# Performance work log

Measured on AMD Instinct MI355X. Metric: run time of the kernel, lower is better.

## Reference

```python
import jax, jax.numpy as jnp
import numpy as np

D_MODEL = 1024
N_HEAD = 16
D_FF = 4 * D_MODEL
LN_EPS = 1e-5


def _layernorm(x, g, b):
    mu = jnp.mean(x, axis=-1, keepdims=True)
    var = jnp.mean(jnp.square(x - mu), axis=-1, keepdims=True)
    return (x - mu) * jax.lax.rsqrt(var + LN_EPS) * g + b


def _mha(q_in, k_in, v_in, mask, wq, bq, wk, wv, bv, wo, bo):
    B, Tq, D = q_in.shape
    H, Dk = N_HEAD, D // N_HEAD
    q = (q_in @ wq + bq).reshape(B, Tq, H, Dk).transpose(0, 2, 1, 3)      # [B,H,Tq,Dk]
    k = (k_in @ wk).reshape(B, -1, H, Dk).transpose(0, 2, 1, 3)           # [B,H,Tk,Dk]
    v = (v_in @ wv + bv).reshape(B, -1, H, Dk).transpose(0, 2, 1, 3)      # [B,H,Tk,Dk]
    attn = jnp.einsum('bhqd,bhkd->bhqk', q, k) / jnp.sqrt(jnp.float32(Dk))
    if mask is not None:
        m0 = (mask[:, None, :, :] == 0)                                    # [B,1,Tq,Tk]
        attn = jnp.where(m0, -jnp.inf, attn)
        attn = jax.nn.softmax(attn, axis=-1)
        attn = jnp.where(m0, 0.0, attn)
    else:
        attn = jax.nn.softmax(attn, axis=-1)
    out = jnp.einsum('bhqk,bhkd->bhqd', attn, v)
    out = out.transpose(0, 2, 1, 3).reshape(B, Tq, D)
    return out @ wo + bo


def setup_inputs() -> dict:
    key = jax.random.key(0)
    ks = jax.random.split(key, 32)
    B, T, S, D = 4, 1024, 1024, D_MODEL
    w = lambda k, shp: 0.02 * jax.random.normal(k, shp, dtype=jnp.float32)
    inp = {
        'dec_input': jax.random.normal(ks[0], (B, T, D), dtype=jnp.float32),
        'enc_output': jax.random.normal(ks[1], (B, S, D), dtype=jnp.float32),
        'self_mask': jnp.broadcast_to(jnp.tril(jnp.ones((T, T), jnp.int32)), (B, T, T)),
        'cross_mask': jnp.ones((B, T, S), jnp.int32),
        'sa_ln_g': jnp.ones((D,), jnp.float32), 'sa_ln_b': jnp.zeros((D,), jnp.float32),
        'sa_wq': w(ks[2], (D, D)), 'sa_bq': jnp.zeros((D,), jnp.float32),
        'sa_wk': w(ks[3], (D, D)),
        'sa_wv': w(ks[4], (D, D)), 'sa_bv': jnp.zeros((D,), jnp.float32),
        'sa_wo': w(ks[5], (D, D)), 'sa_bo': jnp.zeros((D,), jnp.float32),
        'ca_ln_g': jnp.ones((D,), jnp.float32), 'ca_ln_b': jnp.zeros((D,), jnp.float32),
        'ca_wq': w(ks[6], (D, D)), 'ca_bq': jnp.zeros((D,), jnp.float32),
        'ca_wk': w(ks[7], (D, D)),
        'ca_wv': w(ks[8], (D, D)), 'ca_bv': jnp.zeros((D,), jnp.float32),
        'ca_wo': w(ks[9], (D, D)), 'ca_bo': jnp.zeros((D,), jnp.float32),
        'mlp_ln_g': jnp.ones((D,), jnp.float32), 'mlp_ln_b': jnp.zeros((D,), jnp.float32),
        'w1': w(ks[10], (D, D_FF)), 'b1': jnp.zeros((D_FF,), jnp.float32),
        'w2': w(ks[11], (D_FF, D)), 'b2': jnp.zeros((D,), jnp.float32),
    }
    return inp


def reference(dec_input, enc_output, self_mask, cross_mask,
              sa_ln_g, sa_ln_b, sa_wq, sa_bq, sa_wk, sa_wv, sa_bv, sa_wo, sa_bo,
              ca_ln_g, ca_ln_b, ca_wq, ca_bq, ca_wk, ca_wv, ca_bv, ca_wo, ca_bo,
              mlp_ln_g, mlp_ln_b, w1, b1, w2, b2):
    # self-attention block (pre-norm, residual)
    x = _layernorm(dec_input, sa_ln_g, sa_ln_b)
    x = dec_input + _mha(x, x, x, self_mask, sa_wq, sa_bq, sa_wk, sa_wv, sa_bv, sa_wo, sa_bo)
    # cross-attention block
    h = _layernorm(x, ca_ln_g, ca_ln_b)
    x = x + _mha(h, enc_output, enc_output, cross_mask, ca_wq, ca_bq, ca_wk, ca_wv, ca_bv, ca_wo, ca_bo)
    # GELU FFN block
    h = _layernorm(x, mlp_ln_g, mlp_ln_b)
    x = x + (jax.nn.gelu(h @ w1 + b1, approximate=False) @ w2 + b2)
    return x
```

## Files before the change

kernel.cpp:

```cpp
#include <hip/hip_runtime.h>
#include <math.h>

typedef unsigned short u16;
typedef unsigned int   u32;
typedef __attribute__((ext_vector_type(8))) short bf16x8;
typedef __attribute__((ext_vector_type(4))) float f32x4;

__device__ __forceinline__ u16 f2bf(float f) {
  u32 u = __builtin_bit_cast(u32, f);
  u += 0x7fffu + ((u >> 16) & 1u);
  return (u16)(u >> 16);
}

__device__ __forceinline__ void g2l16(const u16* g, u16* l) {
  __builtin_amdgcn_global_load_lds(
      (const __attribute__((address_space(1))) unsigned int*)g,
      (__attribute__((address_space(3))) unsigned int*)l, 16, 0, 0);
}

struct TC8 { const float* s[8]; u16* d[8]; };
__global__ __launch_bounds__(256)
void transcvt8_kernel(TC8 p) {
  const float* __restrict__ W = p.s[blockIdx.z];
  u16* __restrict__ Wt = p.d[blockIdx.z];
  __shared__ float tile[32][33];
  const int n0 = blockIdx.x * 32, k0 = blockIdx.y * 32;
  const int tx = threadIdx.x & 31, ty = threadIdx.x >> 5;
  for (int i = 0; i < 4; ++i)
    tile[ty + 8 * i][tx] = W[(size_t)(k0 + ty + 8 * i) * 1024 + n0 + tx];
  __syncthreads();
  for (int i = 0; i < 4; ++i)
    Wt[(size_t)(n0 + ty + 8 * i) * 1024 + k0 + tx] = f2bf(tile[tx][ty + 8 * i]);
}

__global__ __launch_bounds__(256)
void transcvt_kernel(const float* __restrict__ W, u16* __restrict__ Wt, int K, int N) {
  __shared__ float tile[32][33];
  const int n0 = blockIdx.x * 32, k0 = blockIdx.y * 32;
  const int tx = threadIdx.x & 31, ty = threadIdx.x >> 5;
  for (int i = 0; i < 4; ++i)
    tile[ty + 8 * i][tx] = W[(size_t)(k0 + ty + 8 * i) * N + n0 + tx];
  __syncthreads();
  for (int i = 0; i < 4; ++i)
    Wt[(size_t)(n0 + ty + 8 * i) * K + k0 + tx] = f2bf(tile[tx][ty + 8 * i]);
}

__global__ __launch_bounds__(256)
void cvt_kernel(const float* __restrict__ in, u16* __restrict__ out) {
  const int i = blockIdx.x * 256 + threadIdx.x;
  const float4 v = ((const float4*)in)[i];
  u16 o[4] = {f2bf(v.x), f2bf(v.y), f2bf(v.z), f2bf(v.w)};
  ((ushort4*)out)[i] = *(ushort4*)o;
}

__global__ __launch_bounds__(256)
void pack_bias_kernel(const float* __restrict__ bq, const float* __restrict__ bv,
                      const float* __restrict__ cbv,
                      float* __restrict__ B3, float* __restrict__ B2) {
  const int i = blockIdx.x * 256 + threadIdx.x;
  if (i < 3072) {
    float v = 0.0f;
    if (i < 1024) v = bq[i];
    else if (i >= 2048) v = bv[i - 2048];
    B3[i] = v;
  } else {
    const int j = i - 3072;
    B2[j] = (j >= 1024) ? cbv[j - 1024] : 0.0f;
  }
}

__global__ __launch_bounds__(256)
void ln_kernel(const float* __restrict__ x, const float* __restrict__ g,
               const float* __restrict__ b, u16* __restrict__ out) {
  const int row = blockIdx.x;
  const float4 v4 = ((const float4*)(x + (size_t)row * 1024))[threadIdx.x];
  float vv[4] = {v4.x, v4.y, v4.z, v4.w};
  float s = vv[0] + vv[1] + vv[2] + vv[3];
  float s2 = vv[0] * vv[0] + vv[1] * vv[1] + vv[2] * vv[2] + vv[3] * vv[3];
  for (int m = 1; m < 64; m <<= 1) { s += __shfl_xor(s, m); s2 += __shfl_xor(s2, m); }
  __shared__ float ss[4], ss2[4];
  const int w = threadIdx.x >> 6;
  if ((threadIdx.x & 63) == 0) { ss[w] = s; ss2[w] = s2; }
  __syncthreads();
  s = ss[0] + ss[1] + ss[2] + ss[3];
  s2 = ss2[0] + ss2[1] + ss2[2] + ss2[3];
  const float mu = s * (1.0f / 1024.0f);
  const float var = s2 * (1.0f / 1024.0f) - mu * mu;
  const float r = rsqrtf(var + 1e-5f);
  const int c = threadIdx.x * 4;
  const float4 g4 = ((const float4*)g)[threadIdx.x];
  const float4 b4 = ((const float4*)b)[threadIdx.x];
  float gg[4] = {g4.x, g4.y, g4.z, g4.w};
  float bb[4] = {b4.x, b4.y, b4.z, b4.w};
  u16 o[4];
  for (int j = 0; j < 4; ++j) o[j] = f2bf((vv[j] - mu) * r * gg[j] + bb[j]);
  ((ushort4*)(out + (size_t)row * 1024 + c))[0] = *(ushort4*)o;
}

template<bool RES_F32, bool GELU>
__global__ __launch_bounds__(512)
void gemm_kernel(const u16* __restrict__ A, const u16* __restrict__ Bt,
                 const float* __restrict__ bias, const float* __restrict__ res,
                 void* __restrict__ Cout, int M, int N, int K) {
  __shared__ u16 As[2][128][32];
  __shared__ u16 Bs[2][128][32];
  const int t = threadIdx.x, lane = t & 63, w = t >> 6;
  const int wr = w >> 2, wc = w & 3;
  const int nwg = gridDim.x * gridDim.y;
  int bid = blockIdx.y * gridDim.x + blockIdx.x;
  bid = (bid & 7) * (nwg >> 3) + (bid >> 3);
  const int m0 = (bid / gridDim.x) * 128, n0 = (bid % gridDim.x) * 128;
  const int fr = lane & 15, fg = lane >> 4;
  const int srow = lane >> 2, scol = (lane & 3) * 8;
  const u16* Ag = &A[(size_t)(m0 + w * 16 + srow) * K + scol];
  const u16* Bg = &Bt[(size_t)(n0 + w * 16 + srow) * K + scol];
  f32x4 acc[4][2] = {};
  g2l16(Ag, &As[0][w * 16][0]);
  g2l16(Bg, &Bs[0][w * 16][0]);
  __syncthreads();
  int cur = 0;
  for (int k0 = 0; k0 < K; k0 += 32) {
    if (k0 + 32 < K) {
      const int nx = cur ^ 1, kn = k0 + 32;
      g2l16(Ag + kn, &As[nx][w * 16][0]);
      g2l16(Bg + kn, &Bs[nx][w * 16][0]);
    }
    bf16x8 af[4], bfr[2];
    for (int m = 0; m < 4; ++m) af[m] = *(bf16x8*)&As[cur][wr * 64 + m * 16 + fr][fg * 8];
    for (int n = 0; n < 2; ++n) bfr[n] = *(bf16x8*)&Bs[cur][wc * 32 + n * 16 + fr][fg * 8];
    __builtin_amdgcn_s_setprio(1);
    for (int m = 0; m < 4; ++m)
      for (int n = 0; n < 2; ++n)
        acc[m][n] = __builtin_amdgcn_mfma_f32_16x16x32_bf16(af[m], bfr[n], acc[m][n], 0, 0, 0);
    __builtin_amdgcn_s_setprio(0);
    __syncthreads();
    cur ^= 1;
  }
  for (int m = 0; m < 4; ++m)
    for (int n = 0; n < 2; ++n) {
      const int col = n0 + wc * 32 + n * 16 + fr;
      const float bv = bias ? bias[col] : 0.0f;
      for (int i = 0; i < 4; ++i) {
        const int row = m0 + wr * 64 + m * 16 + fg * 4 + i;
        float v = acc[m][n][i] + bv;
        if (GELU) v = 0.5f * v * (1.0f + erff(v * 0.70710678118654752f));
        if (RES_F32)
          ((float*)Cout)[(size_t)row * N + col] = res[(size_t)row * N + col] + v;
        else
          ((u16*)Cout)[(size_t)row * N + col] = f2bf(v);
      }
    }
}

template<bool CAUSAL>
__global__ __launch_bounds__(256)
void attn_kernel(const u16* __restrict__ Q, int ldq,
                 const u16* __restrict__ K, int ldk,
                 const u16* __restrict__ V, int ldv,
                 u16* __restrict__ O) {
  __shared__ u16 VsT[64][72];
  __shared__ u16 Ps[4][16][72];
  const int bh = blockIdx.y, b = bh >> 4, h = bh & 15;
  const int q0 = blockIdx.x * 64;
  const int t = threadIdx.x;
  const int w = t >> 6, lane = t & 63;
  const int fr = lane & 15, fg = lane >> 4;
  const int qr = q0 + w * 16;
  const int hcol = h * 64;
  const size_t qrow = (size_t)(b * 1024 + qr + fr);
  bf16x8 qf[2];
  qf[0] = *(const bf16x8*)&Q[qrow * ldq + hcol + fg * 8];
  qf[1] = *(const bf16x8*)&Q[qrow * ldq + hcol + 32 + fg * 8];
  f32x4 o[4] = {};
  float mrow[4], lrow[4] = {};
  for (int i = 0; i < 4; ++i) mrow[i] = -1e30f;
  const int vp = t >> 3, vc8 = (t & 7) * 8;
  const int nkt = CAUSAL ? (blockIdx.x + 1) : 16;
  for (int kt = 0; kt < nkt; ++kt) {
    const int k0 = kt * 64;
    {
      const bf16x8 va = *(const bf16x8*)&V[(size_t)(b * 1024 + k0 + 2 * vp) * ldv + hcol + vc8];
      const bf16x8 vb = *(const bf16x8*)&V[(size_t)(b * 1024 + k0 + 2 * vp + 1) * ldv + hcol + vc8];
      #pragma unroll
      for (int j = 0; j < 8; ++j) {
        u16 pair[2] = {((const u16*)&va)[j], ((const u16*)&vb)[j]};
        *(u32*)&VsT[vc8 + j][2 * vp] = *(u32*)pair;
      }
    }
    __syncthreads();
    f32x4 s[4] = {};
    {
      #pragma unroll
      for (int kk = 0; kk < 2; ++kk) {
        bf16x8 kf[4];
        #pragma unroll
        for (int j = 0; j < 4; ++j)
          kf[j] = *(const bf16x8*)&K[(size_t)(b * 1024 + k0 + j * 16 + fr) * ldk + hcol + kk * 32 + fg * 8];
        __builtin_amdgcn_s_setprio(1);
        #pragma unroll
        for (int j = 0; j < 4; ++j)
          s[j] = __builtin_amdgcn_mfma_f32_16x16x32_bf16(qf[kk], kf[j], s[j], 0, 0, 0);
        __builtin_amdgcn_s_setprio(0);
      }
    }
    float p[4][4], rm[4];
    const bool domask = CAUSAL && (kt == nkt - 1);
    for (int i = 0; i < 4; ++i) rm[i] = -1e30f;
    #pragma unroll
    for (int j = 0; j < 4; ++j)
      for (int i = 0; i < 4; ++i) {
        float a = s[j][i] * 0.125f;
        if (domask) {
          const int myq = qr + fg * 4 + i;
          if (k0 + j * 16 + fr > myq) a = -1e30f;
        }
        p[j][i] = a;
        rm[i] = fmaxf(rm[i], a);
      }
    for (int off = 1; off < 16; off <<= 1)
      for (int i = 0; i < 4; ++i) rm[i] = fmaxf(rm[i], __shfl_xor(rm[i], off));
    float rs[4];
    for (int i = 0; i < 4; ++i) {
      const float mn = fmaxf(mrow[i], rm[i]);
      const float sc = __expf(mrow[i] - mn);
      float acc = 0.0f;
      #pragma unroll
      for (int j = 0; j < 4; ++j) { p[j][i] = __expf(p[j][i] - mn); acc += p[j][i]; }
      mrow[i] = mn;
      lrow[i] *= sc;
      rs[i] = acc;
      for (int nb = 0; nb < 4; ++nb) o[nb][i] *= sc;
    }
    for (int off = 1; off < 16; off <<= 1)
      for (int i = 0; i < 4; ++i) rs[i] += __shfl_xor(rs[i], off);
    for (int i = 0; i < 4; ++i) {
      lrow[i] += rs[i];
      #pragma unroll
      for (int j = 0; j < 4; ++j) Ps[w][fg * 4 + i][j * 16 + fr] = f2bf(p[j][i]);
    }
    __syncthreads();
    {
      const bf16x8 pa0 = *(bf16x8*)&Ps[w][fr][fg * 8];
      const bf16x8 pa1 = *(bf16x8*)&Ps[w][fr][32 + fg * 8];
      __builtin_amdgcn_s_setprio(1);
      #pragma unroll
      for (int nb = 0; nb < 4; ++nb) {
        const bf16x8 v0 = *(const bf16x8*)&VsT[nb * 16 + fr][fg * 8];
        const bf16x8 v1 = *(const bf16x8*)&VsT[nb * 16 + fr][32 + fg * 8];
        o[nb] = __builtin_amdgcn_mfma_f32_16x16x32_bf16(pa0, v0, o[nb], 0, 0, 0);
        o[nb] = __builtin_amdgcn_mfma_f32_16x16x32_bf16(pa1, v1, o[nb], 0, 0, 0);
      }
      __builtin_amdgcn_s_setprio(0);
    }
    __syncthreads();
  }
  for (int i = 0; i < 4; ++i) {
    const float inv = 1.0f / lrow[i];
    const size_t row = (size_t)(b * 1024 + qr + fg * 4 + i);
    for (int nb = 0; nb < 4; ++nb)
      O[row * 1024 + hcol + nb * 16 + fr] = f2bf(o[nb][i] * inv);
  }
}

extern "C" void kernel_launch(void* const* d_in, const int* in_sizes, int n_in,
                              void* d_out, int out_size, void* d_ws, size_t ws_size,
                              hipStream_t stream) {
  const float* dec  = (const float*)d_in[0];
  const float* enc  = (const float*)d_in[1];
  const float* sa_g = (const float*)d_in[4];
  const float* sa_b = (const float*)d_in[5];
  const float* sa_wq = (const float*)d_in[6];
  const float* sa_bq = (const float*)d_in[7];
  const float* sa_wk = (const float*)d_in[8];
  const float* sa_wv = (const float*)d_in[9];
  const float* sa_bv = (const float*)d_in[10];
  const float* sa_wo = (const float*)d_in[11];
  const float* sa_bo = (const float*)d_in[12];
  const float* ca_g = (const float*)d_in[13];
  const float* ca_b = (const float*)d_in[14];
  const float* ca_wq = (const float*)d_in[15];
  const float* ca_bq = (const float*)d_in[16];
  const float* ca_wk = (const float*)d_in[17];
  const float* ca_wv = (const float*)d_in[18];
  const float* ca_bv = (const float*)d_in[19];
  const float* ca_wo = (const float*)d_in[20];
  const float* ca_bo = (const float*)d_in[21];
  const float* mlp_g = (const float*)d_in[22];
  const float* mlp_b = (const float*)d_in[23];
  const float* w1 = (const float*)d_in[24];
  const float* b1 = (const float*)d_in[25];
  const float* w2 = (const float*)d_in[26];
  const float* b2 = (const float*)d_in[27];

  const size_t MB = 1024 * 1024;
  if (ws_size < 97 * MB) return;
  char* ws = (char*)d_ws;
  u16* WQKV = (u16*)(ws + 0 * MB);
  u16* CQT  = (u16*)(ws + 6 * MB);
  u16* CKV  = (u16*)(ws + 8 * MB);
  u16* WOT  = (u16*)(ws + 12 * MB);
  u16* COT  = (u16*)(ws + 14 * MB);
  float* B3 = (float*)(ws + 16 * MB);
  float* B2 = (float*)(ws + 16 * MB + 16384);
  u16* XLN  = (u16*)(ws + 17 * MB);
  u16* AO   = (u16*)(ws + 25 * MB);
  u16* W1T  = (u16*)(ws + 25 * MB);
  u16* ENC  = (u16*)(ws + 33 * MB);
  u16* FB   = (u16*)(ws + 41 * MB);
  u16* EF   = (u16*)(ws + 41 * MB);
  u16* CQB  = (u16*)(ws + 57 * MB);
  u16* H1   = (u16*)(ws + 33 * MB);
  float* X1 = (float*)(ws + 65 * MB);
  u16* W2T  = (u16*)(ws + 65 * MB);
  float* X2 = (float*)(ws + 81 * MB);
  float* OUT = (float*)d_out;

  const dim3 blk(256), gblk(512);
  TC8 tc;
  tc.s[0] = sa_wq; tc.d[0] = WQKV;
  tc.s[1] = sa_wk; tc.d[1] = WQKV + 1024 * 1024;
  tc.s[2] = sa_wv; tc.d[2] = WQKV + 2048 * 1024;
  tc.s[3] = sa_wo; tc.d[3] = WOT;
  tc.s[4] = ca_wq; tc.d[4] = CQT;
  tc.s[5] = ca_wk; tc.d[5] = CKV;
  tc.s[6] = ca_wv; tc.d[6] = CKV + 1024 * 1024;
  tc.s[7] = ca_wo; tc.d[7] = COT;
  transcvt8_kernel<<<dim3(32, 32, 8), blk, 0, stream>>>(tc);
  pack_bias_kernel<<<dim3(20), blk, 0, stream>>>(sa_bq, sa_bv, ca_bv, B3, B2);
  cvt_kernel<<<dim3(4096), blk, 0, stream>>>(enc, ENC);

  ln_kernel<<<dim3(4096), blk, 0, stream>>>(dec, sa_g, sa_b, XLN);
  gemm_kernel<false, false><<<dim3(24, 32), gblk, 0, stream>>>(XLN, WQKV, B3, nullptr, FB, 4096, 3072, 1024);
  attn_kernel<true><<<dim3(16, 64), blk, 0, stream>>>(FB, 3072, FB + 1024, 3072, FB + 2048, 3072, AO);
  gemm_kernel<true, false><<<dim3(8, 32), gblk, 0, stream>>>(AO, WOT, sa_bo, dec, X1, 4096, 1024, 1024);

  ln_kernel<<<dim3(4096), blk, 0, stream>>>(X1, ca_g, ca_b, XLN);
  gemm_kernel<false, false><<<dim3(16, 32), gblk, 0, stream>>>(ENC, CKV, B2, nullptr, EF, 4096, 2048, 1024);
  gemm_kernel<false, false><<<dim3(8, 32), gblk, 0, stream>>>(XLN, CQT, ca_bq, nullptr, CQB, 4096, 1024, 1024);
  attn_kernel<false><<<dim3(16, 64), blk, 0, stream>>>(CQB, 1024, EF, 2048, EF + 1024, 2048, AO);
  gemm_kernel<true, false><<<dim3(8, 32), gblk, 0, stream>>>(AO, COT, ca_bo, X1, X2, 4096, 1024, 1024);

  transcvt_kernel<<<dim3(128, 32), blk, 0, stream>>>(w1, W1T, 1024, 4096);
  transcvt_kernel<<<dim3(32, 128), blk, 0, stream>>>(w2, W2T, 4096, 1024);
  ln_kernel<<<dim3(4096), blk, 0, stream>>>(X2, mlp_g, mlp_b, XLN);
  gemm_kernel<false, true><<<dim3(32, 32), gblk, 0, stream>>>(XLN, W1T, b1, nullptr, H1, 4096, 4096, 1024);
  gemm_kernel<true, false><<<dim3(8, 32), gblk, 0, stream>>>(H1, W2T, b2, X2, OUT, 4096, 1024, 4096);
}
```

Before: 455.9 us.

## Restructure attention kernel with double-buffered V, transposed S, and lazy softmax rescale

Rewrites the attention inner loop. The S=QK^T MFMA is computed transposed so each lane owns one query row, which removes the per-row shuffle reductions. V is double-buffered in swizzled LDS with the next tile prefetched into registers during compute, and one barrier per iteration replaces two. The softmax now uses exp2 with a folded scale, skips the rescale when the running max grows by no more than 8, and packs P stores as u32. This cuts synchronization and shuffle overhead, at the cost of more LDS and registers and some subtle lane-mapping correctness risk.

```diff
diff --git a/kernel.cpp b/kernel.cpp
--- a/kernel.cpp
+++ b/kernel.cpp
@@ -10,6 +10,9 @@
   u32 u = __builtin_bit_cast(u32, f);
   u += 0x7fffu + ((u >> 16) & 1u);
   return (u16)(u >> 16);
+}
+__device__ __forceinline__ u32 pack2(float a, float b) {
+  return (u32)f2bf(a) | ((u32)f2bf(b) << 16);
 }
 
 __device__ __forceinline__ void g2l16(const u16* g, u16* l) {
@@ -158,107 +161,132 @@
                  const u16* __restrict__ K, int ldk,
                  const u16* __restrict__ V, int ldv,
                  u16* __restrict__ O) {
-  __shared__ u16 VsT[64][72];
+  __shared__ u16 VsT[2][64][64];
   __shared__ u16 Ps[4][16][72];
   const int bh = blockIdx.y, b = bh >> 4, h = bh & 15;
   const int q0 = blockIdx.x * 64;
-  const int t = threadIdx.x;
-  const int w = t >> 6, lane = t & 63;
-  const int fr = lane & 15, fg = lane >> 4;
+  const int t = threadIdx.x, w = t >> 6, lane = t & 63;
+  const int ql = lane & 15;
+  const int hi = lane >> 4;
   const int qr = q0 + w * 16;
+  const int qz = qr + ql;
   const int hcol = h * 64;
-  const size_t qrow = (size_t)(b * 1024 + qr + fr);
-  bf16x8 qf[2];
-  qf[0] = *(const bf16x8*)&Q[qrow * ldq + hcol + fg * 8];
-  qf[1] = *(const bf16x8*)&Q[qrow * ldq + hcol + 32 + fg * 8];
+  const size_t qgrow = (size_t)(b * 1024 + qz) * ldq + hcol;
+  bf16x8 qb[2];
+  qb[0] = *(const bf16x8*)&Q[qgrow + hi * 8];
+  qb[1] = *(const bf16x8*)&Q[qgrow + 32 + hi * 8];
   f32x4 o[4] = {};
-  float mrow[4], lrow[4] = {};
-  for (int i = 0; i < 4; ++i) mrow[i] = -1e30f;
-  const int vp = t >> 3, vc8 = (t & 7) * 8;
+  float mrow = -1e30f;
+  float lsum = 0.0f;
+  const int sp = t >> 3, sm = t & 7;
+  const float c1 = 0.125f * 1.44269504f;
   const int nkt = CAUSAL ? (blockIdx.x + 1) : 16;
+  {
+    const bf16x8 va = *(const bf16x8*)&V[(size_t)(b * 1024 + 2 * sp) * ldv + hcol + 8 * sm];
+    const bf16x8 vb = *(const bf16x8*)&V[(size_t)(b * 1024 + 2 * sp + 1) * ldv + hcol + 8 * sm];
+    #pragma unroll
+    for (int jj = 0; jj < 8; ++jj) {
+      u32 pr = (u32)((const u16*)&va)[jj] | ((u32)((const u16*)&vb)[jj] << 16);
+      *(u32*)&VsT[0][8 * sm + jj][(2 * sp) ^ ((jj ^ sm) << 3)] = pr;
+    }
+  }
+  __syncthreads();
+  int cur = 0;
   for (int kt = 0; kt < nkt; ++kt) {
     const int k0 = kt * 64;
-    {
-      const bf16x8 va = *(const bf16x8*)&V[(size_t)(b * 1024 + k0 + 2 * vp) * ldv + hcol + vc8];
-      const bf16x8 vb = *(const bf16x8*)&V[(size_t)(b * 1024 + k0 + 2 * vp + 1) * ldv + hcol + vc8];
-      #pragma unroll
-      for (int j = 0; j < 8; ++j) {
-        u16 pair[2] = {((const u16*)&va)[j], ((const u16*)&vb)[j]};
-        *(u32*)&VsT[vc8 + j][2 * vp] = *(u32*)pair;
+    bf16x8 va, vb;
+    const bool havenext = (kt + 1 < nkt);
+    if (havenext) {
+      va = *(const bf16x8*)&V[(size_t)(b * 1024 + k0 + 64 + 2 * sp) * ldv + hcol + 8 * sm];
+      vb = *(const bf16x8*)&V[(size_t)(b * 1024 + k0 + 64 + 2 * sp + 1) * ldv + hcol + 8 * sm];
+    }
+    f32x4 s[4] = {};
+    #pragma unroll
+    for (int kk = 0; kk < 2; ++kk) {
+      bf16x8 kf[4];
+      #pragma unroll
+      for (int j = 0; j < 4; ++j)
+        kf[j] = *(const bf16x8*)&K[(size_t)(b * 1024 + k0 + j * 16 + ql) * ldk + hcol + kk * 32 + hi * 8];
+      __builtin_amdgcn_s_setprio(1);
+      #pragma unroll
+      for (int j = 0; j < 4; ++j)
+        s[j] = __builtin_amdgcn_mfma_f32_16x16x32_bf16(kf[j], qb[kk], s[j], 0, 0, 0);
+      __builtin_amdgcn_s_setprio(0);
+    }
+    float e2[4][4];
+    float rm = -1e30f;
+    const bool domask = CAUSAL && (kt == nkt - 1);
+    #pragma unroll
+    for (int j = 0; j < 4; ++j)
+      #pragma unroll
+      for (int i = 0; i < 4; ++i) {
+        float a = s[j][i] * c1;
+        if (domask && (k0 + j * 16 + hi * 4 + i > qz)) a = -1e30f;
+        e2[j][i] = a;
+        rm = fmaxf(rm, a);
       }
+    if (!__all(rm <= mrow + 8.0f)) {
+      rm = fmaxf(rm, __shfl_xor(rm, 16));
+      rm = fmaxf(rm, __shfl_xor(rm, 32));
+      const float mn = fmaxf(mrow, rm);
+      const float sc = exp2f(mrow - mn);
+      lsum *= sc;
+      float scv[4];
+      #pragma unroll
+      for (int i = 0; i < 4; ++i) scv[i] = __shfl(sc, hi * 4 + i);
+      #pragma unroll
+      for (int nb = 0; nb < 4; ++nb)
+        #pragma unroll
+        for (int i = 0; i < 4; ++i) o[nb][i] *= scv[i];
+      mrow = mn;
+    }
+    float p[4][4];
+    #pragma unroll
+    for (int j = 0; j < 4; ++j)
+      #pragma unroll
+      for (int i = 0; i < 4; ++i) { p[j][i] = exp2f(e2[j][i] - mrow); lsum += p[j][i]; }
+    #pragma unroll
+    for (int j = 0; j < 4; ++j) {
+      *(u32*)&Ps[w][ql][j * 16 + hi * 4]     = pack2(p[j][0], p[j][1]);
+      *(u32*)&Ps[w][ql][j * 16 + hi * 4 + 2] = pack2(p[j][2], p[j][3]);
+    }
+    asm volatile("s_waitcnt lgkmcnt(0)" ::: "memory");
+    __builtin_amdgcn_sched_barrier(0);
+    bf16x8 pa[2];
+    pa[0] = *(const bf16x8*)&Ps[w][ql][hi * 8];
+    pa[1] = *(const bf16x8*)&Ps[w][ql][32 + hi * 8];
+    __builtin_amdgcn_s_setprio(1);
+    #pragma unroll
+    for (int nb = 0; nb < 4; ++nb) {
+      const int dim = nb * 16 + ql;
+      const int swz = ((dim & 7) ^ ((dim >> 3) & 7)) << 3;
+      const bf16x8 v0 = *(const bf16x8*)&VsT[cur][dim][(hi * 8) ^ swz];
+      const bf16x8 v1 = *(const bf16x8*)&VsT[cur][dim][(32 + hi * 8) ^ swz];
+      o[nb] = __builtin_amdgcn_mfma_f32_16x16x32_bf16(pa[0], v0, o[nb], 0, 0, 0);
+      o[nb] = __builtin_amdgcn_mfma_f32_16x16x32_bf16(pa[1], v1, o[nb], 0, 0, 0);
+    }
+    __builtin_amdgcn_s_setprio(0);
+    if (havenext) {
+      const int nx = cur ^ 1;
+      #pragma unroll
+      for (int jj = 0; jj < 8; ++jj) {
+        u32 pr = (u32)((const u16*)&va)[jj] | ((u32)((const u16*)&vb)[jj] << 16);
+        *(u32*)&VsT[nx][8 * sm + jj][(2 * sp) ^ ((jj ^ sm) << 3)] = pr;
+      }
     }
     __syncthreads();
-    f32x4 s[4] = {};
-    {
-      #pragma unroll
-      for (int kk = 0; kk < 2; ++kk) {
-        bf16x8 kf[4];
-        #pragma unroll
-        for (int j = 0; j < 4; ++j)
-          kf[j] = *(const bf16x8*)&K[(size_t)(b * 1024 + k0 + j * 16 + fr) * ldk + hcol + kk * 32 + fg * 8];
-        __builtin_amdgcn_s_setprio(1);
-        #pragma unroll
-        for (int j = 0; j < 4; ++j)
-          s[j] = __builtin_amdgcn_mfma_f32_16x16x32_bf16(qf[kk], kf[j], s[j], 0, 0, 0);
-        __builtin_amdgcn_s_setprio(0);
-      }
-    }
-    float p[4][4], rm[4];
-    const bool domask = CAUSAL && (kt == nkt - 1);
-    for (int i = 0; i < 4; ++i) rm[i] = -1e30f;
-    #pragma unroll
-    for (int j = 0; j < 4; ++j)
-      for (int i = 0; i < 4; ++i) {
-        float a = s[j][i] * 0.125f;
-        if (domask) {
-          const int myq = qr + fg * 4 + i;
-          if (k0 + j * 16 + fr > myq) a = -1e30f;
-        }
-        p[j][i] = a;
-        rm[i] = fmaxf(rm[i], a);
-      }
-    for (int off = 1; off < 16; off <<= 1)
-      for (int i = 0; i < 4; ++i) rm[i] = fmaxf(rm[i], __shfl_xor(rm[i], off));
-    float rs[4];
-    for (int i = 0; i < 4; ++i) {
-      const float mn = fmaxf(mrow[i], rm[i]);
-      const float sc = __expf(mrow[i] - mn);
-      float acc = 0.0f;
-      #pragma unroll
-      for (int j = 0; j < 4; ++j) { p[j][i] = __expf(p[j][i] - mn); acc += p[j][i]; }
-      mrow[i] = mn;
-      lrow[i] *= sc;
-      rs[i] = acc;
-      for (int nb = 0; nb < 4; ++nb) o[nb][i] *= sc;
-    }
-    for (int off = 1; off < 16; off <<= 1)
-      for (int i = 0; i < 4; ++i) rs[i] += __shfl_xor(rs[i], off);
-    for (int i = 0; i < 4; ++i) {
-      lrow[i] += rs[i];
-      #pragma unroll
-      for (int j = 0; j < 4; ++j) Ps[w][fg * 4 + i][j * 16 + fr] = f2bf(p[j][i]);
-    }
-    __syncthreads();
-    {
-      const bf16x8 pa0 = *(bf16x8*)&Ps[w][fr][fg * 8];
-      const bf16x8 pa1 = *(bf16x8*)&Ps[w][fr][32 + fg * 8];
-      __builtin_amdgcn_s_setprio(1);
-      #pragma unroll
-      for (int nb = 0; nb < 4; ++nb) {
-        const bf16x8 v0 = *(const bf16x8*)&VsT[nb * 16 + fr][fg * 8];
-        const bf16x8 v1 = *(const bf16x8*)&VsT[nb * 16 + fr][32 + fg * 8];
-        o[nb] = __builtin_amdgcn_mfma_f32_16x16x32_bf16(pa0, v0, o[nb], 0, 0, 0);
-        o[nb] = __builtin_amdgcn_mfma_f32_16x16x32_bf16(pa1, v1, o[nb], 0, 0, 0);
-      }
-      __builtin_amdgcn_s_setprio(0);
-    }
-    __syncthreads();
-  }
+    cur ^= 1;
+  }
+  float ltot = lsum + __shfl_xor(lsum, 16);
+  ltot += __shfl_xor(ltot, 32);
+  const float inv = 1.0f / ltot;
+  #pragma unroll
   for (int i = 0; i < 4; ++i) {
-    const float inv = 1.0f / lrow[i];
-    const size_t row = (size_t)(b * 1024 + qr + fg * 4 + i);
+    const float invq = __shfl(inv, hi * 4 + i);
+    const size_t row = (size_t)(b * 1024 + qr + hi * 4 + i);
+    #pragma unroll
     for (int nb = 0; nb < 4; ++nb)
-      O[row * 1024 + hcol + nb * 16 + fr] = f2bf(o[nb][i] * inv);
+      O[row * 1024 + hcol + nb * 16 + ql] = f2bf(o[nb][i] * invq);
   }
 }
 
```

Measured after the change: 454.1 us. Within noise of the previous version (-0.4%).
